# Performance work log

Measured on AMD Instinct MI355X. Metric: run time of the kernel, lower is better.

The kernel has to match this reference:

```python
import jax, jax.numpy as jnp
from jax import lax
import numpy as np

B, T, FEAT = 32, 256, 640
H, P = 2048, 640  # lstm_hidden_units, lstm_projection
FORGET_BIAS = 1.0  # TF v1 LSTMCell default


def setup_inputs() -> dict:
    key = jax.random.key(0)
    ks = jax.random.split(key, 6)
    s = 0.02  # small init so tanh/sigmoid stay well-conditioned
    return {
        "x": jax.random.normal(ks[0], (B, T, FEAT), dtype=jnp.float32),
        "W0": jax.random.normal(ks[1], (FEAT + P, 4 * H), dtype=jnp.float32) * s,
        "b0": jnp.zeros((4 * H,), dtype=jnp.float32),
        "P0": jax.random.normal(ks[2], (H, P), dtype=jnp.float32) * s,
        "W1": jax.random.normal(ks[3], (P + P, 4 * H), dtype=jnp.float32) * s,
        "b1": jnp.zeros((4 * H,), dtype=jnp.float32),
        "P1": jax.random.normal(ks[4], (H, P), dtype=jnp.float32) * s,
    }


def _lstmp_layer(x, W, b, proj):
    # x: [B, T, D]; TF v1 LSTMCell with num_proj, gate order (i, j, f, o)
    batch = x.shape[0]
    c0 = jnp.zeros((batch, H), dtype=x.dtype)
    m0 = jnp.zeros((batch, proj.shape[1]), dtype=x.dtype)

    def step(carry, xt):
        c, m = carry
        z = jnp.concatenate([xt, m], axis=-1) @ W + b  # [B, 4H]
        i, j, f, o = jnp.split(z, 4, axis=-1)
        c_new = jax.nn.sigmoid(f + FORGET_BIAS) * c + jax.nn.sigmoid(i) * jnp.tanh(j)
        m_new = (jax.nn.sigmoid(o) * jnp.tanh(c_new)) @ proj  # [B, P]
        return (c_new, m_new), m_new

    xT = jnp.swapaxes(x, 0, 1)  # [T, B, D]
    _, ys = lax.scan(step, (c0, m0), xT)
    return jnp.swapaxes(ys, 0, 1)  # [B, T, P]


def reference(x, W0, b0, P0, W1, b1, P1):
    h = _lstmp_layer(x, W0, b0, P0)
    h = _lstmp_layer(h, W1, b1, P1)
    return h
```

## Files before the change

### kernel.cpp

```cpp
#include <hip/hip_runtime.h>
#include <math.h>

typedef __attribute__((ext_vector_type(8))) short s16x8;
typedef __attribute__((ext_vector_type(8))) _Float16 f16x8;
typedef __attribute__((ext_vector_type(16))) float f32x16;
typedef unsigned long long u64;
typedef unsigned short u16;

#define NBLK 256
#define NTHR 512

constexpr int HSZ2 = 32 * 2048;

__device__ __forceinline__ float sigm(float v) { return 1.0f / (1.0f + expf(-v)); }

__device__ __forceinline__ unsigned short bf16_rne(float x) {
    unsigned u = __float_as_uint(x);
    return (unsigned short)((u + 0x7FFFu + ((u >> 16) & 1u)) >> 16);
}
__device__ __forceinline__ void split2(float x, unsigned short& hi, unsigned short& lo) {
    unsigned u = __float_as_uint(x);
    hi = (unsigned short)(u >> 16);
    float hf = __uint_as_float(u & 0xFFFF0000u);
    lo = bf16_rne(x - hf);
}
__device__ __forceinline__ void split8(const float* f, s16x8& h, s16x8& l) {
    #pragma unroll
    for (int i = 0; i < 8; ++i) {
        unsigned short hh, ll;
        split2(f[i], hh, ll);
        h[i] = (short)hh; l[i] = (short)ll;
    }
}

__device__ __forceinline__ void ast64(u16* p, u64 v) {
    __hip_atomic_store((u64*)p, v, __ATOMIC_RELAXED, __HIP_MEMORY_SCOPE_AGENT);
}

__device__ __forceinline__ void pollall(const unsigned* arr, unsigned e) {
    if (threadIdx.x < 64) {
        const int i0 = (int)threadIdx.x * 4;
        for (;;) {
            bool ok = (__hip_atomic_load(arr + i0 + 0, __ATOMIC_RELAXED, __HIP_MEMORY_SCOPE_AGENT) >= e) &&
                      (__hip_atomic_load(arr + i0 + 1, __ATOMIC_RELAXED, __HIP_MEMORY_SCOPE_AGENT) >= e) &&
                      (__hip_atomic_load(arr + i0 + 2, __ATOMIC_RELAXED, __HIP_MEMORY_SCOPE_AGENT) >= e) &&
                      (__hip_atomic_load(arr + i0 + 3, __ATOMIC_RELAXED, __HIP_MEMORY_SCOPE_AGENT) >= e);
            if (__all(ok)) break;
            __builtin_amdgcn_s_sleep(1);
        }
    }
    __syncthreads();
}

__global__ void transpose_split(const float* __restrict__ in,
                                u16* __restrict__ outHi, u16* __restrict__ outLo,
                                int R, int C) {
    __shared__ float tile[32][33];
    const int c0 = blockIdx.x * 32, r0 = blockIdx.y * 32;
    const int tid = threadIdx.x;
    {
        int r = tid >> 3, q = (tid & 7) * 4;
        float4 v = *(const float4*)(in + (size_t)(r0 + r) * C + c0 + q);
        tile[q + 0][r] = v.x; tile[q + 1][r] = v.y;
        tile[q + 2][r] = v.z; tile[q + 3][r] = v.w;
    }
    __syncthreads();
    {
        int c = tid >> 3, q = (tid & 7) * 4;
        ushort4 h, l;
        unsigned short hh, ll;
        split2(tile[c][q + 0], hh, ll); h.x = hh; l.x = ll;
        split2(tile[c][q + 1], hh, ll); h.y = hh; l.y = ll;
        split2(tile[c][q + 2], hh, ll); h.z = hh; l.z = ll;
        split2(tile[c][q + 3], hh, ll); h.w = hh; l.w = ll;
        size_t o = (size_t)(c0 + c) * R + r0 + q;
        *(ushort4*)(outHi + o) = h;
        *(ushort4*)(outLo + o) = l;
    }
}

__global__ void transpose_f16(const float* __restrict__ in, u16* __restrict__ outp,
                              int R, int C) {
    __shared__ float tile[32][33];
    const int c0 = blockIdx.x * 32, r0 = blockIdx.y * 32;
    const int tid = threadIdx.x;
    {
        int r = tid >> 3, q = (tid & 7) * 4;
        float4 v = *(const float4*)(in + (size_t)(r0 + r) * C + c0 + q);
        tile[q + 0][r] = v.x; tile[q + 1][r] = v.y;
        tile[q + 2][r] = v.z; tile[q + 3][r] = v.w;
    }
    __syncthreads();
    {
        int c = tid >> 3, q = (tid & 7) * 4;
        ushort4 o;
        o.x = __builtin_bit_cast(u16, (_Float16)tile[c][q + 0]);
        o.y = __builtin_bit_cast(u16, (_Float16)tile[c][q + 1]);
        o.z = __builtin_bit_cast(u16, (_Float16)tile[c][q + 2]);
        o.w = __builtin_bit_cast(u16, (_Float16)tile[c][q + 3]);
        *(ushort4*)(outp + (size_t)(c0 + c) * R + r0 + q) = o;
    }
}

__global__ void xcast(const float* __restrict__ in, u16* __restrict__ outp, int n4) {
    int i = blockIdx.x * blockDim.x + threadIdx.x;
    if (i < n4) {
        float4 v = ((const float4*)in)[i];
        ushort4 o;
        o.x = __builtin_bit_cast(u16, (_Float16)v.x);
        o.y = __builtin_bit_cast(u16, (_Float16)v.y);
        o.z = __builtin_bit_cast(u16, (_Float16)v.z);
        o.w = __builtin_bit_cast(u16, (_Float16)v.w);
        ((ushort4*)outp)[i] = o;
    }
}

__global__ void __launch_bounds__(256) qgemm(const float* __restrict__ P,
    const u16* __restrict__ WH, const u16* __restrict__ WL,
    u16* __restrict__ Qt, int rowOff) {
    const int tid = threadIdx.x;
    const int wid = tid >> 6, lane = tid & 63;
    const int n = lane & 31, kg = lane >> 5;
    const int tile = blockIdx.x * 4 + wid;
    const int ct = tile & 255, kt = tile >> 8;
    const int col = ct * 32 + n;
    const int krow = kt * 32 + n;

    f32x16 acc;
    #pragma unroll
    for (int r = 0; r < 16; ++r) acc[r] = 0.f;

    const float* ap = P + (size_t)krow * 640 + kg * 8;
    const u16* bhp = WH + (size_t)col * 1280 + rowOff + kg * 8;
    const u16* blp = WL + (size_t)col * 1280 + rowOff + kg * 8;
    #pragma unroll 4
    for (int ks = 0; ks < 40; ++ks) {
        float4 v0 = *(const float4*)(ap + ks * 16);
        float4 v1 = *(const float4*)(ap + ks * 16 + 4);
        float f[8] = {v0.x, v0.y, v0.z, v0.w, v1.x, v1.y, v1.z, v1.w};
        s16x8 ah, al;
        split8(f, ah, al);
        s16x8 bh = *(const s16x8*)(bhp + ks * 16);
        s16x8 bl = *(const s16x8*)(blp + ks * 16);
        acc = __builtin_amdgcn_mfma_f32_32x32x16_bf16(ah, bh, acc, 0, 0, 0);
        acc = __builtin_amdgcn_mfma_f32_32x32x16_bf16(ah, bl, acc, 0, 0, 0);
        acc = __builtin_amdgcn_mfma_f32_32x32x16_bf16(al, bh, acc, 0, 0, 0);
    }
    u16* qrow = Qt + (size_t)col * 2048 + kt * 32 + 4 * kg;
    #pragma unroll
    for (int q = 0; q < 4; ++q) {
        ushort4 o;
        o.x = __builtin_bit_cast(u16, (_Float16)acc[4 * q + 0]);
        o.y = __builtin_bit_cast(u16, (_Float16)acc[4 * q + 1]);
        o.z = __builtin_bit_cast(u16, (_Float16)acc[4 * q + 2]);
        o.w = __builtin_bit_cast(u16, (_Float16)acc[4 * q + 3]);
        *(ushort4*)(qrow + 8 * q) = o;
    }
}

__global__ void __launch_bounds__(NTHR, 1) lstm_pipe(
    const u16* __restrict__ xh,
    const float* __restrict__ bias0, const float* __restrict__ bias1,
    const u16* __restrict__ Wxt0,
    const u16* __restrict__ Qt0, const u16* __restrict__ Qt01, const u16* __restrict__ Qt1,
    const u16* __restrict__ Pt1,
    u16* __restrict__ hb0, u16* __restrict__ hb1,
    float* out, unsigned* arr) {
    __shared__ float part[8][64][20];
    __shared__ float zb0[32][33];
    __shared__ float zb1[32][33];
    __shared__ u16 hst0[32][8];
    __shared__ u16 hst1[32][8];

    const int tid = threadIdx.x, bid = blockIdx.x;
    const int wid = tid >> 6, lane = tid & 63;
    const int n = lane & 31, kg = lane >> 5;

    const int colmap = (n >> 3) * 2048 + bid * 8 + (n & 7);
    const size_t wx640 = (size_t)colmap * 640 + wid * 80 + kg * 8;
    const size_t qOff  = (size_t)colmap * 2048 + wid * 256 + kg * 8;
    const size_t aXh   = (size_t)n * (256 * 640) + wid * 80 + kg * 8;
    const size_t hROff = (size_t)n * 2048 + wid * 256 + kg * 8;

    const int rn = tid >> 4, rm0 = (tid & 15) * 2;
    const int ch = tid >> 5, cb = tid & 31;

    const bool isT = bid < 40;
    const int  tb  = (bid < 20) ? bid : bid - 20;
    const int  par = (bid < 20) ? 0 : 1;
    const size_t pOff = (size_t)(tb * 32 + n) * 2048 + wid * 256 + kg * 8;

    const float bv0 = bias0[(rn >> 3) * 2048 + bid * 8 + (rn & 7)];
    const float bv1 = bias1[(rn >> 3) * 2048 + bid * 8 + (rn & 7)];

    uint4 q0r[16], q01r[16], q1r[16];
    #pragma unroll
    for (int ks = 0; ks < 16; ++ks) {
        q0r[ks]  = *(const uint4*)(Qt0  + qOff + ks * 16);
        q01r[ks] = *(const uint4*)(Qt01 + qOff + ks * 16);
        q1r[ks]  = *(const uint4*)(Qt1  + qOff + ks * 16);
    }
    #pragma unroll
    for (int ks = 0; ks < 16; ++ks) {
        asm volatile("" : "+v"(q0r[ks].x),  "+v"(q0r[ks].y),  "+v"(q0r[ks].z),  "+v"(q0r[ks].w));
        asm volatile("" : "+v"(q01r[ks].x), "+v"(q01r[ks].y), "+v"(q01r[ks].z), "+v"(q01r[ks].w));
        asm volatile("" : "+v"(q1r[ks].x),  "+v"(q1r[ks].y),  "+v"(q1r[ks].z),  "+v"(q1r[ks].w));
    }

    float creg0 = 0.f, creg1 = 0.f;

    auto xp0 = [&](int t) -> f32x16 {
        f32x16 a;
        #pragma unroll
        for (int r = 0; r < 16; ++r) a[r] = 0.f;
        const u16* xb = xh + aXh + (size_t)t * 640;
        const u16* wb = Wxt0 + wx640;
        #pragma unroll
        for (int ks = 0; ks < 5; ++ks)
            a = __builtin_amdgcn_mfma_f32_32x32x16_f16(*(const f16x8*)(xb + ks * 16),
                                                       *(const f16x8*)(wb + ks * 16), a, 0, 0, 0);
        return a;
    };
    auto stash = [&](const f32x16& v) {
        #pragma unroll
        for (int r = 0; r < 4; ++r) {
            float4 w;
            w.x = v[4 * r + 0]; w.y = v[4 * r + 1];
            w.z = v[4 * r + 2]; w.w = v[4 * r + 3];
            *(float4*)&part[wid][lane][4 * r] = w;
        }
    };
    auto sum8 = [&](int m) -> float {
        int lp = rn + 32 * ((m >> 2) & 1);
        int rg = (m & 3) + 4 * (m >> 3);
        float s = 0.f;
        #pragma unroll
        for (int w = 0; w < 8; ++w) s += part[w][lp][rg];
        return s;
    };

    f32x16 zacc0 = xp0(0);

    for (int g = 0; g <= 257; ++g) {
        if (g > 0) pollall(arr, (unsigned)g);
        const int s = g - 1;
        const bool doL0 = (g <= 255);
        const bool doL1 = (s >= 0 && s <= 255);

        f32x16 acc0, acc1;
        if (doL0) acc0 = zacc0;
        if (doL1) {
            #pragma unroll
            for (int r = 0; r < 16; ++r) acc1[r] = 0.f;
        }
        if (g >= 1) {
            const u16* h0c = hb0 + (size_t)(g - 1) * HSZ2 + hROff;
            if (doL0 && doL1) {
                #pragma unroll
                for (int ks = 0; ks < 16; ++ks) {
                    f16x8 a = *(const f16x8*)(h0c + ks * 16);
                    acc0 = __builtin_amdgcn_mfma_f32_32x32x16_f16(a, __builtin_bit_cast(f16x8, q0r[ks]),  acc0, 0, 0, 0);
                    acc1 = __builtin_amdgcn_mfma_f32_32x32x16_f16(a, __builtin_bit_cast(f16x8, q01r[ks]), acc1, 0, 0, 0);
                }
            } else if (doL0) {
                #pragma unroll
                for (int ks = 0; ks < 16; ++ks)
                    acc0 = __builtin_amdgcn_mfma_f32_32x32x16_f16(*(const f16x8*)(h0c + ks * 16),
                                                                  __builtin_bit_cast(f16x8, q0r[ks]), acc0, 0, 0, 0);
            } else if (doL1) {
                #pragma unroll
                for (int ks = 0; ks < 16; ++ks)
                    acc1 = __builtin_amdgcn_mfma_f32_32x32x16_f16(*(const f16x8*)(h0c + ks * 16),
                                                                  __builtin_bit_cast(f16x8, q01r[ks]), acc1, 0, 0, 0);
            }
        }
        if (s >= 1) {
            const u16* h1c = hb1 + (size_t)(s - 1) * HSZ2 + hROff;
            #pragma unroll
            for (int ks = 0; ks < 16; ++ks)
                acc1 = __builtin_amdgcn_mfma_f32_32x32x16_f16(*(const f16x8*)(h1c + ks * 16),
                                                              __builtin_bit_cast(f16x8, q1r[ks]), acc1, 0, 0, 0);
        }

        if (doL0) {
            stash(acc0);
            __syncthreads();
            #pragma unroll
            for (int j = 0; j < 2; ++j) { int m = rm0 + j; zb0[rn][m] = sum8(m) + bv0; }
        }
        __syncthreads();
        if (doL1) {
            stash(acc1);
            __syncthreads();
            #pragma unroll
            for (int j = 0; j < 2; ++j) { int m = rm0 + j; zb1[rn][m] = sum8(m) + bv1; }
        }
        if (doL0 && tid < 256) {
            float zi = zb0[0 * 8 + ch][cb];
            float zj = zb0[1 * 8 + ch][cb];
            float zf = zb0[2 * 8 + ch][cb];
            float zo = zb0[3 * 8 + ch][cb];
            float cn = sigm(zf + 1.0f) * creg0 + sigm(zi) * tanhf(zj);
            creg0 = cn;
            hst0[cb][ch] = __builtin_bit_cast(u16, (_Float16)(sigm(zo) * tanhf(cn)));
        }
        __syncthreads();
        if (doL1 && tid < 256) {
            float zi = zb1[0 * 8 + ch][cb];
            float zj = zb1[1 * 8 + ch][cb];
            float zf = zb1[2 * 8 + ch][cb];
            float zo = zb1[3 * 8 + ch][cb];
            float cn = sigm(zf + 1.0f) * creg1 + sigm(zi) * tanhf(zj);
            creg1 = cn;
            hst1[cb][ch] = __builtin_bit_cast(u16, (_Float16)(sigm(zo) * tanhf(cn)));
        }
        __syncthreads();

        if (doL0 && wid == 0) {
            int b = tid >> 1, hf = tid & 1;
            u64 v = *(const u64*)&hst0[b][hf * 4];
            ast64(hb0 + (size_t)g * HSZ2 + (size_t)b * 2048 + bid * 8 + hf * 4, v);
        }
        if (doL1 && wid == 1) {
            int l = tid - 64;
            int b = l >> 1, hf = l & 1;
            u64 v = *(const u64*)&hst1[b][hf * 4];
            ast64(hb1 + (size_t)s * HSZ2 + (size_t)b * 2048 + bid * 8 + hf * 4, v);
        }
        __syncthreads();
        if (tid == 0)
            __hip_atomic_store(arr + bid, (unsigned)(g + 1), __ATOMIC_RELAXED, __HIP_MEMORY_SCOPE_AGENT);

        const int sp = g - 2;
        if (isT && sp >= 0 && (sp & 1) == par) {
            f32x16 pacc;
            #pragma unroll
            for (int r = 0; r < 16; ++r) pacc[r] = 0.f;
            const u16* hc = hb1 + (size_t)sp * HSZ2 + hROff;
            const u16* pf = Pt1 + pOff;
            #pragma unroll
            for (int ks = 0; ks < 16; ++ks)
                pacc = __builtin_amdgcn_mfma_f32_32x32x16_f16(*(const f16x8*)(hc + ks * 16),
                                                              *(const f16x8*)(pf + ks * 16), pacc, 0, 0, 0);
            __syncthreads();
            stash(pacc);
            __syncthreads();
            #pragma unroll
            for (int j = 0; j < 2; ++j) {
                int m = rm0 + j;
                out[((size_t)m * 256 + sp) * 640 + tb * 32 + rn] = sum8(m);
            }
        }
        if (g < 255) zacc0 = xp0(g + 1);
    }
}

__device__ __forceinline__ void grid_bar_slow(unsigned int* bar, unsigned int& epoch) {
    __syncthreads();
    epoch++;
    if (threadIdx.x == 0) {
        __threadfence();
        atomicAdd(bar, 1u);
        const unsigned int target = epoch * NBLK;
        while (__hip_atomic_load(bar, __ATOMIC_RELAXED, __HIP_MEMORY_SCOPE_AGENT) < target)
            __builtin_amdgcn_s_sleep(1);
        __threadfence();
    }
    __syncthreads();
}

__global__ void __launch_bounds__(NTHR, 1) lstm_fb(
    const float* __restrict__ x,
    const float* __restrict__ W0, const float* __restrict__ b0, const float* __restrict__ Pr0,
    const float* __restrict__ W1, const float* __restrict__ b1, const float* __restrict__ Pr1,
    float* out, float* ws) {
    const int tid = threadIdx.x;
    const int bid = blockIdx.x;
    unsigned int* bar = (unsigned int*)ws;
    float* mbuf0 = ws + 1024;
    float* mbuf1 = mbuf0 + 32 * 640;
    float* hws = mbuf1 + 32 * 640;
    __shared__ float zbuf[32 * 33];
    __shared__ float pred[512];
    unsigned int epoch = 0;
    const int c_idx = tid & 31;
    const int bg = tid >> 5;
    const int b0r = bg * 2;
    const int col = (c_idx >> 3) * 2048 + bid * 8 + (c_idx & 7);
    const int ch = tid >> 5;
    const int cb = tid & 31;
    const int p_s = (bid * 640) / NBLK;
    const int p_e = ((bid + 1) * 640) / NBLK;
    const int np = p_e - p_s;
    const int kq_n = (np == 2) ? 8 : 4;
    const int klen = 2048 / kq_n;
    const int pg = tid >> 5;
    const bool pact = pg < np * kq_n;
    const int pj = pact ? (pg % np) : 0;
    const int kq = pact ? (pg / np) : 0;
    for (int layer = 0; layer < 2; ++layer) {
        const float* W = layer ? W1 : W0;
        const float* bbv = layer ? b1 : b0;
        const float* Pr = layer ? Pr1 : Pr0;
        const float* inb = layer ? (const float*)out : x;
        for (int i = bid * NTHR + tid; i < 32 * 640; i += NBLK * NTHR) mbuf0[i] = 0.0f;
        float creg = 0.0f;
        grid_bar_slow(bar, epoch);
        const float bias = bbv[col];
        for (int t = 0; t < 256; ++t) {
            float* mcur = (t & 1) ? mbuf1 : mbuf0;
            float* mnxt = (t & 1) ? mbuf0 : mbuf1;
            const float* in0 = inb + (size_t)(b0r * 256 + t) * 640;
            const float* in1 = in0 + (size_t)256 * 640;
            const float* wp = W + col;
            float a0 = 0.f, a1 = 0.f;
            #pragma unroll 4
            for (int k = 0; k < 640; k += 4) {
                float4 u0 = *(const float4*)(in0 + k);
                float4 u1 = *(const float4*)(in1 + k);
                float w0 = wp[(size_t)(k + 0) * 8192], w1 = wp[(size_t)(k + 1) * 8192];
                float w2 = wp[(size_t)(k + 2) * 8192], w3 = wp[(size_t)(k + 3) * 8192];
                a0 += w0 * u0.x + w1 * u0.y + w2 * u0.z + w3 * u0.w;
                a1 += w0 * u1.x + w1 * u1.y + w2 * u1.z + w3 * u1.w;
            }
            const float* q0 = mcur + (size_t)b0r * 640;
            const float* q1 = q0 + 640;
            #pragma unroll 4
            for (int k = 0; k < 640; k += 4) {
                float4 u0 = *(const float4*)(q0 + k);
                float4 u1 = *(const float4*)(q1 + k);
                float w0 = wp[(size_t)(640 + k + 0) * 8192], w1 = wp[(size_t)(640 + k + 1) * 8192];
                float w2 = wp[(size_t)(640 + k + 2) * 8192], w3 = wp[(size_t)(640 + k + 3) * 8192];
                a0 += w0 * u0.x + w1 * u0.y + w2 * u0.z + w3 * u0.w;
                a1 += w0 * u1.x + w1 * u1.y + w2 * u1.z + w3 * u1.w;
            }
            zbuf[c_idx * 33 + b0r + 0] = a0 + bias;
            zbuf[c_idx * 33 + b0r + 1] = a1 + bias;
            __syncthreads();
            if (tid < 256) {
                float zi = zbuf[(0 * 8 + ch) * 33 + cb];
                float zj = zbuf[(1 * 8 + ch) * 33 + cb];
                float zf = zbuf[(2 * 8 + ch) * 33 + cb];
                float zo = zbuf[(3 * 8 + ch) * 33 + cb];
                float cn = sigm(zf + 1.0f) * creg + sigm(zi) * tanhf(zj);
                creg = cn;
                hws[(size_t)(bid * 8 + ch) * 32 + cb] = sigm(zo) * tanhf(cn);
            }
            grid_bar_slow(bar, epoch);
            if (pact) {
                const int p = p_s + pj;
                const float* pp = Pr + p;
                const int k0 = kq * klen;
                float s = 0.f;
                #pragma unroll 4
                for (int k = k0; k < k0 + klen; ++k) s += hws[(size_t)k * 32 + cb] * pp[(size_t)k * 640];
                pred[(pj * 32 + cb) * kq_n + kq] = s;
            }
            __syncthreads();
            if (tid < np * 32) {
                float s = 0.f;
                for (int q2 = 0; q2 < kq_n; ++q2) s += pred[tid * kq_n + q2];
                const int p = p_s + (tid >> 5);
                const int b = tid & 31;
                mnxt[(size_t)b * 640 + p] = s;
                out[((size_t)b * 256 + t) * 640 + p] = s;
            }
            grid_bar_slow(bar, epoch);
        }
    }
}

extern "C" void kernel_launch(void* const* d_in, const int* in_sizes, int n_in,
                              void* d_out, int out_size, void* d_ws, size_t ws_size,
                              hipStream_t stream) {
    const float* x   = (const float*)d_in[0];
    const float* W0  = (const float*)d_in[1];
    const float* b0  = (const float*)d_in[2];
    const float* P0  = (const float*)d_in[3];
    const float* W1  = (const float*)d_in[4];
    const float* b1  = (const float*)d_in[5];
    const float* P1  = (const float*)d_in[6];
    float* out = (float*)d_out;

    size_t off = 0;
    auto alloc = [&](size_t bytes) { size_t o = off; off += (bytes + 255) & ~(size_t)255; return o; };
    const size_t oBar  = alloc(32768);
    const size_t szW   = (size_t)8192 * 1280 * 2;
    const size_t szQ   = (size_t)8192 * 2048 * 2;
    const size_t szPt  = (size_t)640 * 2048 * 2;
    const size_t szWx  = (size_t)8192 * 640 * 2;
    const size_t oWH   = alloc(szW), oWL = alloc(szW);
    const size_t oQt0  = alloc(szQ), oQt01 = alloc(szQ), oQt1 = alloc(szQ);
    const size_t oPt1  = alloc(szPt);
    const size_t oWx0  = alloc(szWx);
    const size_t oXh   = alloc((size_t)32 * 256 * 640 * 2);
    const size_t oH0   = alloc((size_t)256 * HSZ2 * 2);
    const size_t oH1   = alloc((size_t)256 * HSZ2 * 2);
    const size_t need  = off;

    hipMemsetAsync(d_ws, 0, 32768, stream);

    if (ws_size < need) {
        float* ws = (float*)d_ws;
        void* args[] = {(void*)&x, (void*)&W0, (void*)&b0, (void*)&P0,
                        (void*)&W1, (void*)&b1, (void*)&P1, (void*)&out, (void*)&ws};
        hipError_t err = hipLaunchCooperativeKernel((const void*)lstm_fb,
                                                    dim3(NBLK), dim3(NTHR), args, 0, stream);
        if (err != hipSuccess)
            lstm_fb<<<dim3(NBLK), dim3(NTHR), 0, stream>>>(x, W0, b0, P0, W1, b1, P1, out, ws);
        return;
    }

    char* w = (char*)d_ws;
    u16 *WHp = (u16*)(w + oWH), *WLp = (u16*)(w + oWL);
    u16 *Qt0p = (u16*)(w + oQt0), *Qt01p = (u16*)(w + oQt01), *Qt1p = (u16*)(w + oQt1);
    u16 *Pt1p = (u16*)(w + oPt1);
    u16 *Wx0p = (u16*)(w + oWx0);
    u16 *xhp  = (u16*)(w + oXh);
    u16 *hb0p = (u16*)(w + oH0), *hb1p = (u16*)(w + oH1);
    unsigned* arrp = (unsigned*)(w + oBar);

    transpose_split<<<dim3(256, 40), 256, 0, stream>>>(W0, WHp, WLp, 1280, 8192);
    qgemm<<<dim3(4096), 256, 0, stream>>>(P0, WHp, WLp, Qt0p, 640);
    transpose_split<<<dim3(256, 40), 256, 0, stream>>>(W1, WHp, WLp, 1280, 8192);
    qgemm<<<dim3(4096), 256, 0, stream>>>(P0, WHp, WLp, Qt01p, 0);
    qgemm<<<dim3(4096), 256, 0, stream>>>(P1, WHp, WLp, Qt1p, 640);
    transpose_f16<<<dim3(20, 64), 256, 0, stream>>>(P1, Pt1p, 2048, 640);
    transpose_f16<<<dim3(256, 20), 256, 0, stream>>>(W0, Wx0p, 640, 8192);
    xcast<<<dim3(5120), 256, 0, stream>>>(x, xhp, 32 * 256 * 640 / 4);

    const float *b0c = b0, *b1c = b1;
    void* args[] = {(void*)&xhp, (void*)&b0c, (void*)&b1c,
                    (void*)&Wx0p,
                    (void*)&Qt0p, (void*)&Qt01p, (void*)&Qt1p, (void*)&Pt1p,
                    (void*)&hb0p, (void*)&hb1p,
                    (void*)&out, (void*)&arrp};
    hipError_t err = hipLaunchCooperativeKernel((const void*)lstm_pipe,
                                                dim3(NBLK), dim3(NTHR), args, 0, stream);
    if (err != hipSuccess)
        lstm_pipe<<<dim3(NBLK), dim3(NTHR), 0, stream>>>(
            xhp, b0c, b1c, Wx0p, Qt0p, Qt01p, Qt1p, Pt1p, hb0p, hb1p, out, arrp);
}
```

Baseline: 6.281 ms.

## Merge both layers' gate reductions into one phase and defer output projection

```diff
diff --git a/kernel.cpp b/kernel.cpp
--- a/kernel.cpp
+++ b/kernel.cpp
@@ -166,9 +166,8 @@
     const u16* __restrict__ Pt1,
     u16* __restrict__ hb0, u16* __restrict__ hb1,
     float* out, unsigned* arr) {
-    __shared__ float part[8][64][20];
-    __shared__ float zb0[32][33];
-    __shared__ float zb1[32][33];
+    __shared__ float part0[8][64][20];
+    __shared__ float part1[8][64][20];
     __shared__ u16 hst0[32][8];
     __shared__ u16 hst1[32][8];
 
@@ -183,15 +182,16 @@
     const size_t hROff = (size_t)n * 2048 + wid * 256 + kg * 8;
 
     const int rn = tid >> 4, rm0 = (tid & 15) * 2;
-    const int ch = tid >> 5, cb = tid & 31;
-
-    const bool isT = bid < 40;
-    const int  tb  = (bid < 20) ? bid : bid - 20;
-    const int  par = (bid < 20) ? 0 : 1;
-    const size_t pOff = (size_t)(tb * 32 + n) * 2048 + wid * 256 + kg * 8;
-
-    const float bv0 = bias0[(rn >> 3) * 2048 + bid * 8 + (rn & 7)];
-    const float bv1 = bias1[(rn >> 3) * 2048 + bid * 8 + (rn & 7)];
+
+    const bool isC0 = tid < 256;
+    const int cl = tid & 255;
+    const int ch = cl >> 5, cb = cl & 31;
+    float bv[4];
+    #pragma unroll
+    for (int gx = 0; gx < 4; ++gx)
+        bv[gx] = (isC0 ? bias0 : bias1)[gx * 2048 + bid * 8 + ch];
+    const int crg = (cb & 3) + 4 * (cb >> 3);
+    const int clp = 32 * ((cb >> 2) & 1);
 
     uint4 q0r[16], q01r[16], q1r[16];
     #pragma unroll
@@ -207,7 +207,7 @@
         asm volatile("" : "+v"(q1r[ks].x),  "+v"(q1r[ks].y),  "+v"(q1r[ks].z),  "+v"(q1r[ks].w));
     }
 
-    float creg0 = 0.f, creg1 = 0.f;
+    float creg = 0.f;
 
     auto xp0 = [&](int t) -> f32x16 {
         f32x16 a;
@@ -221,31 +221,23 @@
                                                        *(const f16x8*)(wb + ks * 16), a, 0, 0, 0);
         return a;
     };
-    auto stash = [&](const f32x16& v) {
+    auto stash = [&](float (*prt)[64][20], const f32x16& v) {
         #pragma unroll
         for (int r = 0; r < 4; ++r) {
             float4 w;
             w.x = v[4 * r + 0]; w.y = v[4 * r + 1];
             w.z = v[4 * r + 2]; w.w = v[4 * r + 3];
-            *(float4*)&part[wid][lane][4 * r] = w;
+            *(float4*)&prt[wid][lane][4 * r] = w;
         }
     };
-    auto sum8 = [&](int m) -> float {
-        int lp = rn + 32 * ((m >> 2) & 1);
-        int rg = (m & 3) + 4 * (m >> 3);
-        float s = 0.f;
-        #pragma unroll
-        for (int w = 0; w < 8; ++w) s += part[w][lp][rg];
-        return s;
-    };
 
     f32x16 zacc0 = xp0(0);
 
-    for (int g = 0; g <= 257; ++g) {
+    for (int g = 0; g <= 256; ++g) {
         if (g > 0) pollall(arr, (unsigned)g);
         const int s = g - 1;
         const bool doL0 = (g <= 255);
-        const bool doL1 = (s >= 0 && s <= 255);
+        const bool doL1 = (s >= 0);
 
         f32x16 acc0, acc1;
         if (doL0) acc0 = zacc0;
@@ -255,19 +247,14 @@
         }
         if (g >= 1) {
             const u16* h0c = hb0 + (size_t)(g - 1) * HSZ2 + hROff;
-            if (doL0 && doL1) {
+            if (doL0) {
                 #pragma unroll
                 for (int ks = 0; ks < 16; ++ks) {
                     f16x8 a = *(const f16x8*)(h0c + ks * 16);
                     acc0 = __builtin_amdgcn_mfma_f32_32x32x16_f16(a, __builtin_bit_cast(f16x8, q0r[ks]),  acc0, 0, 0, 0);
                     acc1 = __builtin_amdgcn_mfma_f32_32x32x16_f16(a, __builtin_bit_cast(f16x8, q01r[ks]), acc1, 0, 0, 0);
                 }
-            } else if (doL0) {
-                #pragma unroll
-                for (int ks = 0; ks < 16; ++ks)
-                    acc0 = __builtin_amdgcn_mfma_f32_32x32x16_f16(*(const f16x8*)(h0c + ks * 16),
-                                                                  __builtin_bit_cast(f16x8, q0r[ks]), acc0, 0, 0, 0);
-            } else if (doL1) {
+            } else {
                 #pragma unroll
                 for (int ks = 0; ks < 16; ++ks)
                     acc1 = __builtin_amdgcn_mfma_f32_32x32x16_f16(*(const f16x8*)(h0c + ks * 16),
@@ -282,37 +269,25 @@
                                                               __builtin_bit_cast(f16x8, q1r[ks]), acc1, 0, 0, 0);
         }
 
-        if (doL0) {
-            stash(acc0);
-            __syncthreads();
+        if (doL0) stash(part0, acc0);
+        if (doL1) stash(part1, acc1);
+        __syncthreads();
+        if ((isC0 && doL0) || (!isC0 && doL1)) {
+            float (*prt)[64][20] = isC0 ? part0 : part1;
+            float z[4];
             #pragma unroll
-            for (int j = 0; j < 2; ++j) { int m = rm0 + j; zb0[rn][m] = sum8(m) + bv0; }
-        }
-        __syncthreads();
-        if (doL1) {
-            stash(acc1);
-            __syncthreads();
-            #pragma unroll
-            for (int j = 0; j < 2; ++j) { int m = rm0 + j; zb1[rn][m] = sum8(m) + bv1; }
-        }
-        if (doL0 && tid < 256) {
-            float zi = zb0[0 * 8 + ch][cb];
-            float zj = zb0[1 * 8 + ch][cb];
-            float zf = zb0[2 * 8 + ch][cb];
-            float zo = zb0[3 * 8 + ch][cb];
-            float cn = sigm(zf + 1.0f) * creg0 + sigm(zi) * tanhf(zj);
-            creg0 = cn;
-            hst0[cb][ch] = __builtin_bit_cast(u16, (_Float16)(sigm(zo) * tanhf(cn)));
-        }
-        __syncthreads();
-        if (doL1 && tid < 256) {
-            float zi = zb1[0 * 8 + ch][cb];
-            float zj = zb1[1 * 8 + ch][cb];
-            float zf = zb1[2 * 8 + ch][cb];
-            float zo = zb1[3 * 8 + ch][cb];
-            float cn = sigm(zf + 1.0f) * creg1 + sigm(zi) * tanhf(zj);
-            creg1 = cn;
-            hst1[cb][ch] = __builtin_bit_cast(u16, (_Float16)(sigm(zo) * tanhf(cn)));
+            for (int gx = 0; gx < 4; ++gx) {
+                const int lp = (gx * 8 + ch) + clp;
+                float ssum = 0.f;
+                #pragma unroll
+                for (int w = 0; w < 8; ++w) ssum += prt[w][lp][crg];
+                z[gx] = ssum + bv[gx];
+            }
+            float cn = sigm(z[2] + 1.0f) * creg + sigm(z[0]) * tanhf(z[1]);
+            creg = cn;
+            u16 hv = __builtin_bit_cast(u16, (_Float16)(sigm(z[3]) * tanhf(cn)));
+            if (isC0) hst0[cb][ch] = hv;
+            else      hst1[cb][ch] = hv;
         }
         __syncthreads();
 
@@ -331,27 +306,36 @@
         if (tid == 0)
             __hip_atomic_store(arr + bid, (unsigned)(g + 1), __ATOMIC_RELAXED, __HIP_MEMORY_SCOPE_AGENT);
 
-        const int sp = g - 2;
-        if (isT && sp >= 0 && (sp & 1) == par) {
-            f32x16 pacc;
+        if (g < 255) zacc0 = xp0(g + 1);
+    }
+
+    pollall(arr, 257u);
+    const int mb = bid >> 3;
+    const int t0 = (bid * 32) & 255;
+    const size_t aOff = (size_t)(t0 + n) * HSZ2 + (size_t)mb * 2048 + wid * 256 + kg * 8;
+    for (int ct = 0; ct < 20; ++ct) {
+        f32x16 pacc;
+        #pragma unroll
+        for (int r = 0; r < 16; ++r) pacc[r] = 0.f;
+        const u16* ap = hb1 + aOff;
+        const u16* bp = Pt1 + (size_t)(ct * 32 + n) * 2048 + wid * 256 + kg * 8;
+        #pragma unroll
+        for (int ks = 0; ks < 16; ++ks)
+            pacc = __builtin_amdgcn_mfma_f32_32x32x16_f16(*(const f16x8*)(ap + ks * 16),
+                                                          *(const f16x8*)(bp + ks * 16), pacc, 0, 0, 0);
+        __syncthreads();
+        stash(part0, pacc);
+        __syncthreads();
+        #pragma unroll
+        for (int j = 0; j < 2; ++j) {
+            int m = rm0 + j;
+            int lp = rn + 32 * ((m >> 2) & 1);
+            int rg = (m & 3) + 4 * (m >> 3);
+            float ssum = 0.f;
             #pragma unroll
-            for (int r = 0; r < 16; ++r) pacc[r] = 0.f;
-            const u16* hc = hb1 + (size_t)sp * HSZ2 + hROff;
-            const u16* pf = Pt1 + pOff;
-            #pragma unroll
-            for (int ks = 0; ks < 16; ++ks)
-                pacc = __builtin_amdgcn_mfma_f32_32x32x16_f16(*(const f16x8*)(hc + ks * 16),
-                                                              *(const f16x8*)(pf + ks * 16), pacc, 0, 0, 0);
-            __syncthreads();
-            stash(pacc);
-            __syncthreads();
-            #pragma unroll
-            for (int j = 0; j < 2; ++j) {
-                int m = rm0 + j;
-                out[((size_t)m * 256 + sp) * 640 + tb * 32 + rn] = sum8(m);
-            }
-        }
-        if (g < 255) zacc0 = xp0(g + 1);
+            for (int w = 0; w < 8; ++w) ssum += part0[w][lp][rg];
+            out[(size_t)(bid * 32 + m) * 640 + ct * 32 + rn] = ssum;
+        }
     }
 }
 
```

Result: faster. 5.246 ms (-16.5%).
